# Performance work log

Measured on AMD Instinct MI355X. Metric: run time of the kernel, lower is better.

Reference implementation:

```python
import jax, jax.numpy as jnp
import numpy as np

N_NODES = 50000
N_EDGES = 800000
HEADS = 4
OUT_CH = 64
NEG_SLOPE = 0.2  # PyG GATConv default


def gat_conv(x, edge_index, W, att_src, att_dst, bias):
    """PyG GATConv (concat=True, add_self_loops=True, eval mode).
    x: [N, F_in], edge_index: [2, E] (row 0 = src, row 1 = dst).
    W: [F_in, H*C], att_src/att_dst: [1, H, C], bias: [H*C].
    """
    n = x.shape[0]
    loops = jnp.arange(n, dtype=edge_index.dtype)
    src = jnp.concatenate([edge_index[0], loops])  # [E+N]
    dst = jnp.concatenate([edge_index[1], loops])

    h = (x @ W).reshape(n, HEADS, OUT_CH)           # [N, H, C]
    a_src = jnp.sum(h * att_src, axis=-1)           # [N, H]
    a_dst = jnp.sum(h * att_dst, axis=-1)           # [N, H]

    e = a_src[src] + a_dst[dst]                     # [E+N, H]
    e = jax.nn.leaky_relu(e, NEG_SLOPE)

    # segment softmax over incoming edges of each dst node
    e_max = jax.ops.segment_max(e, dst, num_segments=n)   # [N, H]
    e_exp = jnp.exp(e - e_max[dst])
    denom = jax.ops.segment_sum(e_exp, dst, num_segments=n)
    alpha = e_exp / (denom[dst] + 1e-16)            # [E+N, H]

    msg = h[src] * alpha[:, :, None]                # [E+N, H, C]
    out = jax.ops.segment_sum(msg, dst, num_segments=n)   # [N, H, C]
    return out.reshape(n, HEADS * OUT_CH) + bias


def setup_inputs() -> dict:
    key = jax.random.key(0)
    ks = jax.random.split(key, 10)
    d_in = 256
    d_hid = HEADS * OUT_CH  # 256
    s_in = 1.0 / np.sqrt(d_in)
    s_hid = 1.0 / np.sqrt(d_hid)
    return {
        "x": jax.random.normal(ks[0], (N_NODES, d_in), dtype=jnp.float32),
        "edge_index": jax.random.randint(ks[1], (2, N_EDGES), 0, N_NODES, dtype=jnp.int32),
        "W1": jax.random.normal(ks[2], (d_in, d_hid), dtype=jnp.float32) * s_in,
        "att_src1": jax.random.normal(ks[3], (1, HEADS, OUT_CH), dtype=jnp.float32) * s_hid,
        "att_dst1": jax.random.normal(ks[4], (1, HEADS, OUT_CH), dtype=jnp.float32) * s_hid,
        "b1": jnp.zeros((d_hid,), dtype=jnp.float32),
        "W2": jax.random.normal(ks[5], (d_hid, d_hid), dtype=jnp.float32) * s_hid,
        "att_src2": jax.random.normal(ks[6], (1, HEADS, OUT_CH), dtype=jnp.float32) * s_hid,
        "att_dst2": jax.random.normal(ks[7], (1, HEADS, OUT_CH), dtype=jnp.float32) * s_hid,
        "b2": jnp.zeros((d_hid,), dtype=jnp.float32),
    }


def reference(x, edge_index, W1, att_src1, att_dst1, b1, W2, att_src2, att_dst2, b2):
    # layer 1 + ELU (dropout is identity in eval mode)
    h = gat_conv(x, edge_index, W1, att_src1, att_dst1, b1)
    h = jax.nn.elu(h)
    # layer 2 + ELU
    h = gat_conv(h, edge_index, W2, att_src2, att_dst2, b2)
    h = jax.nn.elu(h)
    return h
```

## Files before the change

### kernel.cpp

```cpp
#include <hip/hip_runtime.h>
#include <hip/hip_bf16.h>

#define N_NODES 50000
#define N_EDGES 800000

typedef __attribute__((ext_vector_type(8))) short short8;
typedef __attribute__((ext_vector_type(4))) float floatx4;
typedef __attribute__((ext_vector_type(2))) uint uintx2;

__device__ __forceinline__ ushort f2bf(float f) {
    uint u = __float_as_uint(f);
    uint r = u + 0x7FFFu + ((u >> 16) & 1u);
    return (ushort)(r >> 16);
}
__device__ __forceinline__ float bfu2f(ushort h) {
    return __uint_as_float(((uint)h) << 16);
}
__device__ __forceinline__ float bflo(uint u) { return __uint_as_float(u << 16); }
__device__ __forceinline__ float bfhi(uint u) { return __uint_as_float(u & 0xffff0000u); }
__device__ __forceinline__ float lrelu(float e) { return e >= 0.f ? e : 0.2f * e; }

__global__ void deg_kernel(const int* __restrict__ dst, int* __restrict__ cnt, int E) {
    int i = blockIdx.x * blockDim.x + threadIdx.x;
    if (i < E) atomicAdd(&cnt[dst[i]], 1);
}

__global__ __launch_bounds__(256) void scan1_kernel(const int* __restrict__ cnt,
                                                    int* __restrict__ excl,
                                                    int* __restrict__ partial, int n) {
    __shared__ int sd[256];
    int tid = threadIdx.x;
    int i = blockIdx.x * 256 + tid;
    int v = (i < n) ? cnt[i] : 0;
    sd[tid] = v;
    __syncthreads();
    #pragma unroll
    for (int off = 1; off < 256; off <<= 1) {
        int t = (tid >= off) ? sd[tid - off] : 0;
        __syncthreads();
        sd[tid] += t;
        __syncthreads();
    }
    if (i < n) excl[i] = sd[tid] - v;
    if (tid == 255) partial[blockIdx.x] = sd[255];
}

__global__ __launch_bounds__(256) void scan2_kernel(int* __restrict__ partial, int nb) {
    __shared__ int sd[256];
    int tid = threadIdx.x;
    int v = (tid < nb) ? partial[tid] : 0;
    sd[tid] = v;
    __syncthreads();
    #pragma unroll
    for (int off = 1; off < 256; off <<= 1) {
        int t = (tid >= off) ? sd[tid - off] : 0;
        __syncthreads();
        sd[tid] += t;
        __syncthreads();
    }
    if (tid < nb) partial[tid] = sd[tid] - v;
}

__global__ __launch_bounds__(256) void scan3_kernel(const int* __restrict__ excl,
                                                    const int* __restrict__ partial,
                                                    int* __restrict__ row_ptr,
                                                    int* __restrict__ row_tmp, int n) {
    int i = blockIdx.x * 256 + threadIdx.x;
    if (i < n) {
        int v = excl[i] + partial[blockIdx.x];
        row_ptr[i] = v;
        row_tmp[i] = v;
    }
    if (i == 0) row_ptr[n] = N_EDGES;
}

__global__ void scatter_kernel(const int* __restrict__ src, const int* __restrict__ dst,
                               int* __restrict__ row_tmp, int* __restrict__ sorted_src,
                               int* __restrict__ sorted_dst, int E) {
    int i = blockIdx.x * blockDim.x + threadIdx.x;
    if (i < E) {
        int d = dst[i];
        int p = atomicAdd(&row_tmp[d], 1);
        sorted_src[p] = src[i];
        sorted_dst[p] = d;
    }
}

__global__ __launch_bounds__(320) void prep_w(const float* __restrict__ W1,
                                              const float* __restrict__ W2,
                                              const float* __restrict__ as1,
                                              const float* __restrict__ ad1,
                                              const float* __restrict__ as2,
                                              const float* __restrict__ ad2,
                                              ushort* __restrict__ Wt1_hi,
                                              ushort* __restrict__ Wt1_lo,
                                              ushort* __restrict__ Wt2_hi,
                                              ushort* __restrict__ Wt2_lo) {
    int t = threadIdx.x, k = blockIdx.x & 255;
    int l1 = (blockIdx.x < 256);
    const float* W = l1 ? W1 : W2;
    const float* as_ = l1 ? as1 : as2;
    const float* ad_ = l1 ? ad1 : ad2;
    ushort* Wh = l1 ? Wt1_hi : Wt2_hi;
    ushort* Wl = l1 ? Wt1_lo : Wt2_lo;
    if (t < 256) {
        float v = W[k * 256 + t];
        ushort hb = f2bf(v);
        Wh[t * 256 + k] = hb;
        Wl[t * 256 + k] = f2bf(v - bfu2f(hb));
    } else if (t < 264) {
        int j = t - 256;
        int h = j & 3;
        const float* vec = (j < 4) ? as_ : ad_;
        float acc = 0.f;
        for (int c = 0; c < 64; c++) acc += W[k * 256 + h * 64 + c] * vec[h * 64 + c];
        ushort hb = f2bf(acc);
        Wh[t * 256 + k] = hb;
        Wl[t * 256 + k] = f2bf(acc - bfu2f(hb));
    } else if (t < 272) {
        Wh[t * 256 + k] = 0;
        Wl[t * 256 + k] = 0;
    }
}

__global__ __launch_bounds__(256) void gemm_att_kernel(const float* __restrict__ A,
                                                       const ushort* __restrict__ Wt_hi,
                                                       const ushort* __restrict__ Wt_lo,
                                                       const float* __restrict__ att_s,
                                                       const float* __restrict__ att_d,
                                                       ushort* __restrict__ H,
                                                       float* __restrict__ a_src,
                                                       float* __restrict__ a_dst, int M) {
    const int ROWP = 40;
    __shared__ ushort hi_s[2][128 * ROWP];
    __shared__ ushort lo_s[2][128 * ROWP];
    const int tid = threadIdx.x;
    const int wave = tid >> 6, lane = tid & 63;
    const int quad = lane >> 4, l16 = lane & 15;
    const int brow = blockIdx.x * 64;
    const int coff = blockIdx.y * 128;
    const int mrow = brow + wave * 16 + l16;
    const int mload = (mrow < M) ? mrow : (M - 1);

    floatx4 acc[8];
    #pragma unroll
    for (int t = 0; t < 8; t++) acc[t] = (floatx4){0.f, 0.f, 0.f, 0.f};

    const int scol = tid & 127;
    const ushort* gW = ((tid < 128) ? Wt_hi : Wt_lo) + (size_t)(coff + scol) * 256;
    ushort* sB0 = ((tid < 128) ? &hi_s[0][0] : &lo_s[0][0]) + scol * ROWP;
    ushort* sB1 = ((tid < 128) ? &hi_s[1][0] : &lo_s[1][0]) + scol * ROWP;

    const float* ap = A + (size_t)mload * 256 + quad * 8;

    short8 wreg[4];
    #pragma unroll
    for (int i = 0; i < 4; i++)
        wreg[i] = *reinterpret_cast<const short8*>(gW + i * 8);
    float4 af0[2], af1[2];
    af0[0] = *reinterpret_cast<const float4*>(ap);
    af1[0] = *reinterpret_cast<const float4*>(ap + 4);
    af0[1] = *reinterpret_cast<const float4*>(ap + 32);
    af1[1] = *reinterpret_cast<const float4*>(ap + 36);
    #pragma unroll
    for (int i = 0; i < 4; i++)
        *reinterpret_cast<short8*>(sB0 + i * 8) = wreg[i];
    asm volatile("s_waitcnt lgkmcnt(0)" ::: "memory");
    __builtin_amdgcn_s_barrier();

    #pragma unroll
    for (int t = 0; t < 8; t++) {
        const int cur = t & 1;
        if (t < 7) {
            #pragma unroll
            for (int i = 0; i < 4; i++)
                wreg[i] = *reinterpret_cast<const short8*>(gW + (t + 1) * 32 + i * 8);
        }
        float av[8] = {af0[cur].x, af0[cur].y, af0[cur].z, af0[cur].w,
                       af1[cur].x, af1[cur].y, af1[cur].z, af1[cur].w};
        short8 a_hi, a_lo;
        #pragma unroll
        for (int j = 0; j < 8; j++) {
            ushort hb = f2bf(av[j]);
            a_hi[j] = (short)hb;
            a_lo[j] = (short)f2bf(av[j] - bfu2f(hb));
        }
        if (t < 6) {
            af0[cur] = *reinterpret_cast<const float4*>(ap + (t + 2) * 32);
            af1[cur] = *reinterpret_cast<const float4*>(ap + (t + 2) * 32 + 4);
        }
        const ushort* rh = (cur == 0) ? &hi_s[0][0] : &hi_s[1][0];
        const ushort* rl = (cur == 0) ? &lo_s[0][0] : &lo_s[1][0];
        #pragma unroll
        for (int tt = 0; tt < 8; tt++) {
            int roff = (tt * 16 + l16) * ROWP + quad * 8;
            short8 b_hi = *reinterpret_cast<const short8*>(rh + roff);
            short8 b_lo = *reinterpret_cast<const short8*>(rl + roff);
            acc[tt] = __builtin_amdgcn_mfma_f32_16x16x32_bf16(a_hi, b_hi, acc[tt], 0, 0, 0);
            acc[tt] = __builtin_amdgcn_mfma_f32_16x16x32_bf16(a_hi, b_lo, acc[tt], 0, 0, 0);
            acc[tt] = __builtin_amdgcn_mfma_f32_16x16x32_bf16(a_lo, b_hi, acc[tt], 0, 0, 0);
        }
        if (t < 7) {
            ushort* sBn = cur ? sB0 : sB1;
            #pragma unroll
            for (int i = 0; i < 4; i++)
                *reinterpret_cast<short8*>(sBn + i * 8) = wreg[i];
        }
        asm volatile("s_waitcnt lgkmcnt(0)" ::: "memory");
        __builtin_amdgcn_s_barrier();
    }
    const int hb = blockIdx.y * 2;
    float ps[2][4] = {}, pd[2][4] = {};
    #pragma unroll
    for (int t = 0; t < 8; t++) {
        int hh = t >> 2;
        float as_v = att_s[coff + t * 16 + l16];
        float ad_v = att_d[coff + t * 16 + l16];
        #pragma unroll
        for (int r = 0; r < 4; r++) {
            ps[hh][r] += acc[t][r] * as_v;
            pd[hh][r] += acc[t][r] * ad_v;
        }
    }
    #pragma unroll
    for (int off = 1; off < 16; off <<= 1) {
        #pragma unroll
        for (int hh = 0; hh < 2; hh++)
            #pragma unroll
            for (int r = 0; r < 4; r++) {
                ps[hh][r] += __shfl_xor(ps[hh][r], off, 64);
                pd[hh][r] += __shfl_xor(pd[hh][r], off, 64);
            }
    }
    if (l16 == 0) {
        #pragma unroll
        for (int r = 0; r < 4; r++) {
            int m = brow + wave * 16 + quad * 4 + r;
            if (m < M) {
                #pragma unroll
                for (int hh = 0; hh < 2; hh++) {
                    a_src[m * 4 + hb + hh] = ps[hh][r];
                    a_dst[m * 4 + hb + hh] = pd[hh][r];
                }
            }
        }
    }
    #pragma unroll
    for (int t = 0; t < 4; t++) {
        int c = t * 16 + l16;
        #pragma unroll
        for (int r = 0; r < 4; r++) {
            int m = brow + wave * 16 + quad * 4 + r;
            if (m < M) {
                uint pk = (uint)f2bf(acc[t][r]) | ((uint)f2bf(acc[t + 4][r]) << 16);
                *reinterpret_cast<uint*>(H + (size_t)m * 256 + c * 4 + hb) = pk;
            }
        }
    }
}

__global__ __launch_bounds__(256) void ew_kernel(const float* __restrict__ a_src,
                                                 const float* __restrict__ a_dst,
                                                 const int* __restrict__ sorted_src,
                                                 const int* __restrict__ sorted_dst,
                                                 float* __restrict__ ew, int E) {
    int j = blockIdx.x * 256 + threadIdx.x;
    if (j >= E) return;
    int s = sorted_src[j], d = sorted_dst[j];
    float4 as_ = *reinterpret_cast<const float4*>(a_src + (size_t)s * 4);
    float4 ad_ = *reinterpret_cast<const float4*>(a_dst + (size_t)d * 4);
    float4 w;
    w.x = __expf(lrelu(as_.x + ad_.x));
    w.y = __expf(lrelu(as_.y + ad_.y));
    w.z = __expf(lrelu(as_.z + ad_.z));
    w.w = __expf(lrelu(as_.w + ad_.w));
    *reinterpret_cast<float4*>(ew + (size_t)j * 4) = w;
}

#define AGG_ACC(W_, V_)                                                     \
    do {                                                                    \
        a0 += (W_).x * bflo((V_).x); a1 += (W_).y * bfhi((V_).x);           \
        a2 += (W_).z * bflo((V_).y); a3 += (W_).w * bfhi((V_).y);           \
        dp0 += (W_).x; dp1 += (W_).y; dp2 += (W_).z; dp3 += (W_).w;         \
    } while (0)

__global__ __launch_bounds__(256) void agg_kernel(const ushort* __restrict__ H,
                                                  const float* __restrict__ a_src,
                                                  const float* __restrict__ a_dst,
                                                  const int* __restrict__ row_ptr,
                                                  const int* __restrict__ sorted_src,
                                                  const float* __restrict__ ew,
                                                  const float* __restrict__ bias,
                                                  float* __restrict__ out, int N) {
    const int lane = threadIdx.x & 63;
    const int i = __builtin_amdgcn_readfirstlane(blockIdx.x * 4 + (threadIdx.x >> 6));
    if (i >= N) return;
    const float4 asv = *reinterpret_cast<const float4*>(a_src + (size_t)i * 4);
    const float4 adv = *reinterpret_cast<const float4*>(a_dst + (size_t)i * 4);
    const float ws0 = __expf(lrelu(asv.x + adv.x)), ws1 = __expf(lrelu(asv.y + adv.y));
    const float ws2 = __expf(lrelu(asv.z + adv.z)), ws3 = __expf(lrelu(asv.w + adv.w));
    const int start = row_ptr[i], end = row_ptr[i + 1];

    float a0 = 0.f, a1 = 0.f, a2 = 0.f, a3 = 0.f;
    float dp0 = 0.f, dp1 = 0.f, dp2 = 0.f, dp3 = 0.f;
    const ushort* __restrict__ Hl = H + lane * 4;

    for (int j0 = start; j0 < end; j0 += 8) {
        int s[8];
        #pragma unroll
        for (int k = 0; k < 8; k++) s[k] = sorted_src[j0 + k];
        floatx4 w[8];
        #pragma unroll
        for (int k = 0; k < 8; k++)
            w[k] = *reinterpret_cast<const floatx4*>(ew + (size_t)(j0 + k) * 4);
        uintx2 hv[8];
        #pragma unroll
        for (int k = 0; k < 8; k++)
            hv[k] = *reinterpret_cast<const uintx2*>(Hl + (size_t)s[k] * 256);
        if (j0 + 8 <= end) {
            #pragma unroll
            for (int k = 0; k < 8; k++) AGG_ACC(w[k], hv[k]);
        } else {
            #pragma unroll
            for (int k = 0; k < 8; k++)
                if (j0 + k < end) AGG_ACC(w[k], hv[k]);
        }
    }
    {
        uintx2 hv = *reinterpret_cast<const uintx2*>(Hl + (size_t)i * 256);
        a0 += ws0 * bflo(hv.x); a1 += ws1 * bfhi(hv.x);
        a2 += ws2 * bflo(hv.y); a3 += ws3 * bfhi(hv.y);
    }
    const float r0 = 1.f / (dp0 + ws0 + 1e-16f), r1 = 1.f / (dp1 + ws1 + 1e-16f);
    const float r2 = 1.f / (dp2 + ws2 + 1e-16f), r3 = 1.f / (dp3 + ws3 + 1e-16f);
    float* op = out + (size_t)i * 256 + lane;
    float v;
    v = a0 * r0 + bias[lane];        v = (v > 0.f) ? v : expm1f(v);
    __builtin_nontemporal_store(v, op);
    v = a1 * r1 + bias[64 + lane];   v = (v > 0.f) ? v : expm1f(v);
    __builtin_nontemporal_store(v, op + 64);
    v = a2 * r2 + bias[128 + lane];  v = (v > 0.f) ? v : expm1f(v);
    __builtin_nontemporal_store(v, op + 128);
    v = a3 * r3 + bias[192 + lane];  v = (v > 0.f) ? v : expm1f(v);
    __builtin_nontemporal_store(v, op + 192);
}

extern "C" void kernel_launch(void* const* d_in, const int* in_sizes, int n_in,
                              void* d_out, int out_size, void* d_ws, size_t ws_size,
                              hipStream_t stream) {
    const float* x      = (const float*)d_in[0];
    const int*   eidx   = (const int*)d_in[1];
    const float* W1     = (const float*)d_in[2];
    const float* att_s1 = (const float*)d_in[3];
    const float* att_d1 = (const float*)d_in[4];
    const float* b1     = (const float*)d_in[5];
    const float* W2     = (const float*)d_in[6];
    const float* att_s2 = (const float*)d_in[7];
    const float* att_d2 = (const float*)d_in[8];
    const float* b2     = (const float*)d_in[9];
    float* out = (float*)d_out;

    const int N = N_NODES, E = N_EDGES;
    char* ws = (char*)d_ws;
    size_t off = 0;
    auto alloc = [&](size_t bytes) -> void* {
        void* p = ws + off;
        off += (bytes + 255) & ~(size_t)255;
        return p;
    };
    ushort* h       = (ushort*)alloc((size_t)N * 256 * sizeof(ushort));
    float*  ew      = (float*) alloc((size_t)E * 4 * sizeof(float));
    float*  a_src   = (float*) alloc((size_t)N * 4 * sizeof(float));
    float*  a_dst   = (float*) alloc((size_t)N * 4 * sizeof(float));
    int*    cnt     = (int*)   alloc((size_t)N * sizeof(int));
    int*    row_ptr = (int*)   alloc((size_t)(N + 1) * sizeof(int));
    int*    row_tmp = (int*)   alloc((size_t)N * sizeof(int));
    int*    sorted  = (int*)   alloc((size_t)E * sizeof(int));
    int*    sortedd = (int*)   alloc((size_t)E * sizeof(int));
    int*    excl    = (int*)   alloc((size_t)N * sizeof(int));
    int*    partial = (int*)   alloc(256 * sizeof(int));
    ushort* Wt1_hi  = (ushort*)alloc(272 * 256 * sizeof(ushort));
    ushort* Wt1_lo  = (ushort*)alloc(272 * 256 * sizeof(ushort));
    ushort* Wt2_hi  = (ushort*)alloc(272 * 256 * sizeof(ushort));
    ushort* Wt2_lo  = (ushort*)alloc(272 * 256 * sizeof(ushort));
    float*  x2      = out;
    (void)ws_size; (void)in_sizes; (void)n_in; (void)out_size;

    const int* e_src = eidx;
    const int* e_dst = eidx + E;
    const int nsb = (N + 255) / 256;
    const int neb = (E + 255) / 256;

    prep_w<<<512, 320, 0, stream>>>(W1, W2, att_s1, att_d1, att_s2, att_d2,
                                    Wt1_hi, Wt1_lo, Wt2_hi, Wt2_lo);
    hipMemsetAsync(cnt, 0, N * sizeof(int), stream);
    deg_kernel<<<neb, 256, 0, stream>>>(e_dst, cnt, E);
    scan1_kernel<<<nsb, 256, 0, stream>>>(cnt, excl, partial, N);
    scan2_kernel<<<1, 256, 0, stream>>>(partial, nsb);
    scan3_kernel<<<nsb, 256, 0, stream>>>(excl, partial, row_ptr, row_tmp, N);
    scatter_kernel<<<neb, 256, 0, stream>>>(e_src, e_dst, row_tmp, sorted, sortedd, E);

    dim3 ggrid((N + 63) / 64, 2);
    int nblk = (N + 3) / 4;
    gemm_att_kernel<<<ggrid, 256, 0, stream>>>(x, Wt1_hi, Wt1_lo, att_s1, att_d1,
                                               h, a_src, a_dst, N);
    ew_kernel<<<neb, 256, 0, stream>>>(a_src, a_dst, sorted, sortedd, ew, E);
    agg_kernel<<<nblk, 256, 0, stream>>>(h, a_src, a_dst, row_ptr, sorted, ew, b1, x2, N);
    gemm_att_kernel<<<ggrid, 256, 0, stream>>>(x2, Wt2_hi, Wt2_lo, att_s2, att_d2,
                                               h, a_src, a_dst, N);
    ew_kernel<<<neb, 256, 0, stream>>>(a_src, a_dst, sorted, sortedd, ew, E);
    agg_kernel<<<nblk, 256, 0, stream>>>(h, a_src, a_dst, row_ptr, sorted, ew, b2, out, N);
}
```

Before: 450.2 us.

## Fuse edge-weight computation into aggregation kernel and drop sorted_dst buffer

Removes the separate ew_kernel and its E*4 float buffer. Each wave now computes the per-edge attention weights inside agg_kernel: every lane handles one (edge, head) pair for 16 edges and broadcasts the weights with shuffles. The sorted_dst array and its writes in scatter go away. The unroll rises from 8 to 16 edges per iteration. This saves two kernel launches and the write and re-read of the edge-weight array, at the cost of extra shuffles, more registers and an a_src gather inside the aggregation loop.

```diff
diff --git a/kernel.cpp b/kernel.cpp
--- a/kernel.cpp
+++ b/kernel.cpp
@@ -76,13 +76,12 @@
 
 __global__ void scatter_kernel(const int* __restrict__ src, const int* __restrict__ dst,
                                int* __restrict__ row_tmp, int* __restrict__ sorted_src,
-                               int* __restrict__ sorted_dst, int E) {
+                               int E) {
     int i = blockIdx.x * blockDim.x + threadIdx.x;
     if (i < E) {
         int d = dst[i];
         int p = atomicAdd(&row_tmp[d], 1);
         sorted_src[p] = src[i];
-        sorted_dst[p] = d;
     }
 }
 
@@ -259,73 +258,72 @@
     }
 }
 
-__global__ __launch_bounds__(256) void ew_kernel(const float* __restrict__ a_src,
-                                                 const float* __restrict__ a_dst,
-                                                 const int* __restrict__ sorted_src,
-                                                 const int* __restrict__ sorted_dst,
-                                                 float* __restrict__ ew, int E) {
-    int j = blockIdx.x * 256 + threadIdx.x;
-    if (j >= E) return;
-    int s = sorted_src[j], d = sorted_dst[j];
-    float4 as_ = *reinterpret_cast<const float4*>(a_src + (size_t)s * 4);
-    float4 ad_ = *reinterpret_cast<const float4*>(a_dst + (size_t)d * 4);
-    float4 w;
-    w.x = __expf(lrelu(as_.x + ad_.x));
-    w.y = __expf(lrelu(as_.y + ad_.y));
-    w.z = __expf(lrelu(as_.z + ad_.z));
-    w.w = __expf(lrelu(as_.w + ad_.w));
-    *reinterpret_cast<float4*>(ew + (size_t)j * 4) = w;
-}
-
-#define AGG_ACC(W_, V_)                                                     \
-    do {                                                                    \
-        a0 += (W_).x * bflo((V_).x); a1 += (W_).y * bfhi((V_).x);           \
-        a2 += (W_).z * bflo((V_).y); a3 += (W_).w * bfhi((V_).y);           \
-        dp0 += (W_).x; dp1 += (W_).y; dp2 += (W_).z; dp3 += (W_).w;         \
-    } while (0)
-
 __global__ __launch_bounds__(256) void agg_kernel(const ushort* __restrict__ H,
                                                   const float* __restrict__ a_src,
                                                   const float* __restrict__ a_dst,
                                                   const int* __restrict__ row_ptr,
                                                   const int* __restrict__ sorted_src,
-                                                  const float* __restrict__ ew,
                                                   const float* __restrict__ bias,
                                                   float* __restrict__ out, int N) {
     const int lane = threadIdx.x & 63;
     const int i = __builtin_amdgcn_readfirstlane(blockIdx.x * 4 + (threadIdx.x >> 6));
     if (i >= N) return;
-    const float4 asv = *reinterpret_cast<const float4*>(a_src + (size_t)i * 4);
-    const float4 adv = *reinterpret_cast<const float4*>(a_dst + (size_t)i * 4);
-    const float ws0 = __expf(lrelu(asv.x + adv.x)), ws1 = __expf(lrelu(asv.y + adv.y));
-    const float ws2 = __expf(lrelu(asv.z + adv.z)), ws3 = __expf(lrelu(asv.w + adv.w));
+    const float4 asvi = *reinterpret_cast<const float4*>(a_src + (size_t)i * 4);
+    const float4 advi = *reinterpret_cast<const float4*>(a_dst + (size_t)i * 4);
+    const float ws0 = __expf(lrelu(asvi.x + advi.x)), ws1 = __expf(lrelu(asvi.y + advi.y));
+    const float ws2 = __expf(lrelu(asvi.z + advi.z)), ws3 = __expf(lrelu(asvi.w + advi.w));
+    const int l3 = lane & 3, lq = lane >> 2;
+    const float advec = (l3 == 0) ? advi.x : (l3 == 1) ? advi.y
+                        : (l3 == 2) ? advi.z : advi.w;
     const int start = row_ptr[i], end = row_ptr[i + 1];
 
-    float a0 = 0.f, a1 = 0.f, a2 = 0.f, a3 = 0.f;
-    float dp0 = 0.f, dp1 = 0.f, dp2 = 0.f, dp3 = 0.f;
+    float a0 = 0.f, a1 = 0.f, a2 = 0.f, a3 = 0.f, dpv = 0.f;
     const ushort* __restrict__ Hl = H + lane * 4;
 
-    for (int j0 = start; j0 < end; j0 += 8) {
-        int s[8];
-        #pragma unroll
-        for (int k = 0; k < 8; k++) s[k] = sorted_src[j0 + k];
-        floatx4 w[8];
-        #pragma unroll
-        for (int k = 0; k < 8; k++)
-            w[k] = *reinterpret_cast<const floatx4*>(ew + (size_t)(j0 + k) * 4);
-        uintx2 hv[8];
-        #pragma unroll
-        for (int k = 0; k < 8; k++)
-            hv[k] = *reinterpret_cast<const uintx2*>(Hl + (size_t)s[k] * 256);
-        if (j0 + 8 <= end) {
-            #pragma unroll
-            for (int k = 0; k < 8; k++) AGG_ACC(w[k], hv[k]);
+    for (int j0 = start; j0 < end; j0 += 16) {
+        int s[16];
+        #pragma unroll
+        for (int k = 0; k < 16; k++) s[k] = sorted_src[j0 + k];
+        int idxv = sorted_src[j0 + lq];
+        float e = a_src[(size_t)idxv * 4 + l3] + advec;
+        float w = __expf(fmaxf(e, 0.2f * e));
+        if (j0 + 16 <= end) {
+            uintx2 hv[16];
+            #pragma unroll
+            for (int k = 0; k < 16; k++)
+                hv[k] = *reinterpret_cast<const uintx2*>(Hl + (size_t)s[k] * 256);
+            dpv += w;
+            #pragma unroll
+            for (int k = 0; k < 16; k++) {
+                float w0 = __shfl(w, 4 * k, 64),     w1 = __shfl(w, 4 * k + 1, 64);
+                float w2 = __shfl(w, 4 * k + 2, 64), w3 = __shfl(w, 4 * k + 3, 64);
+                a0 += w0 * bflo(hv[k].x); a1 += w1 * bfhi(hv[k].x);
+                a2 += w2 * bflo(hv[k].y); a3 += w3 * bfhi(hv[k].y);
+            }
         } else {
-            #pragma unroll
-            for (int k = 0; k < 8; k++)
-                if (j0 + k < end) AGG_ACC(w[k], hv[k]);
-        }
-    }
+            const int nv = end - j0;
+            dpv += (lq < nv) ? w : 0.f;
+            uintx2 hv[16];
+            #pragma unroll
+            for (int k = 0; k < 16; k++)
+                if (k < nv)
+                    hv[k] = *reinterpret_cast<const uintx2*>(Hl + (size_t)s[k] * 256);
+            #pragma unroll
+            for (int k = 0; k < 16; k++)
+                if (k < nv) {
+                    float w0 = __shfl(w, 4 * k, 64),     w1 = __shfl(w, 4 * k + 1, 64);
+                    float w2 = __shfl(w, 4 * k + 2, 64), w3 = __shfl(w, 4 * k + 3, 64);
+                    a0 += w0 * bflo(hv[k].x); a1 += w1 * bfhi(hv[k].x);
+                    a2 += w2 * bflo(hv[k].y); a3 += w3 * bfhi(hv[k].y);
+                }
+        }
+    }
+    dpv += __shfl_xor(dpv, 4, 64);
+    dpv += __shfl_xor(dpv, 8, 64);
+    dpv += __shfl_xor(dpv, 16, 64);
+    dpv += __shfl_xor(dpv, 32, 64);
+    float dp0 = __shfl(dpv, 0, 64), dp1 = __shfl(dpv, 1, 64);
+    float dp2 = __shfl(dpv, 2, 64), dp3 = __shfl(dpv, 3, 64);
     {
         uintx2 hv = *reinterpret_cast<const uintx2*>(Hl + (size_t)i * 256);
         a0 += ws0 * bflo(hv.x); a1 += ws1 * bfhi(hv.x);
@@ -369,14 +367,12 @@
         return p;
     };
     ushort* h       = (ushort*)alloc((size_t)N * 256 * sizeof(ushort));
-    float*  ew      = (float*) alloc((size_t)E * 4 * sizeof(float));
     float*  a_src   = (float*) alloc((size_t)N * 4 * sizeof(float));
     float*  a_dst   = (float*) alloc((size_t)N * 4 * sizeof(float));
+    int*    sorted  = (int*)   alloc((size_t)E * sizeof(int));
     int*    cnt     = (int*)   alloc((size_t)N * sizeof(int));
     int*    row_ptr = (int*)   alloc((size_t)(N + 1) * sizeof(int));
     int*    row_tmp = (int*)   alloc((size_t)N * sizeof(int));
-    int*    sorted  = (int*)   alloc((size_t)E * sizeof(int));
-    int*    sortedd = (int*)   alloc((size_t)E * sizeof(int));
     int*    excl    = (int*)   alloc((size_t)N * sizeof(int));
     int*    partial = (int*)   alloc(256 * sizeof(int));
     ushort* Wt1_hi  = (ushort*)alloc(272 * 256 * sizeof(ushort));
@@ -398,16 +394,14 @@
     scan1_kernel<<<nsb, 256, 0, stream>>>(cnt, excl, partial, N);
     scan2_kernel<<<1, 256, 0, stream>>>(partial, nsb);
     scan3_kernel<<<nsb, 256, 0, stream>>>(excl, partial, row_ptr, row_tmp, N);
-    scatter_kernel<<<neb, 256, 0, stream>>>(e_src, e_dst, row_tmp, sorted, sortedd, E);
+    scatter_kernel<<<neb, 256, 0, stream>>>(e_src, e_dst, row_tmp, sorted, E);
 
     dim3 ggrid((N + 63) / 64, 2);
     int nblk = (N + 3) / 4;
     gemm_att_kernel<<<ggrid, 256, 0, stream>>>(x, Wt1_hi, Wt1_lo, att_s1, att_d1,
                                                h, a_src, a_dst, N);
-    ew_kernel<<<neb, 256, 0, stream>>>(a_src, a_dst, sorted, sortedd, ew, E);
-    agg_kernel<<<nblk, 256, 0, stream>>>(h, a_src, a_dst, row_ptr, sorted, ew, b1, x2, N);
+    agg_kernel<<<nblk, 256, 0, stream>>>(h, a_src, a_dst, row_ptr, sorted, b1, x2, N);
     gemm_att_kernel<<<ggrid, 256, 0, stream>>>(x2, Wt2_hi, Wt2_lo, att_s2, att_d2,
                                                h, a_src, a_dst, N);
-    ew_kernel<<<neb, 256, 0, stream>>>(a_src, a_dst, sorted, sortedd, ew, E);
-    agg_kernel<<<nblk, 256, 0, stream>>>(h, a_src, a_dst, row_ptr, sorted, ew, b2, out, N);
-}
+    agg_kernel<<<nblk, 256, 0, stream>>>(h, a_src, a_dst, row_ptr, sorted, b2, out, N);
+}
```

Measured after the change: 462.3 us. 2.7% more time.
